# Optimization experiments

Measured on AMD Instinct MI355X. Metric: run time of the kernel, lower is better.

Reference implementation:

```python
import jax, jax.numpy as jnp
import numpy as np

N_NODES = 100000  # graph size (set via set_features/adj_lists in the original)
DEGREE = 32       # sampled neighbors per node (num_sample)
N_PAIRS = 8192    # link-prediction batch
FEAT_DIM = 9      # nn.Embedding(18, 9)
HID = 20          # enc1 embed_dim
OUT = 15          # n_out / enc2 embed_dim


def setup_inputs() -> dict:
    key = jax.random.key(0)
    ks = jax.random.split(key, 9)
    to_pred = jax.random.randint(ks[0], (N_PAIRS, 2), 0, N_NODES)
    adj = jax.random.randint(ks[1], (N_NODES, DEGREE), 0, N_NODES)
    feat = jax.random.normal(ks[2], (N_NODES, FEAT_DIM), dtype=jnp.float32)
    W1 = jax.random.normal(ks[3], (HID, 2 * FEAT_DIM), dtype=jnp.float32) * 0.1
    W2 = jax.random.normal(ks[4], (OUT, HID), dtype=jnp.float32) * 0.1
    fc1_w = jax.random.normal(ks[5], (15, 30), dtype=jnp.float32) * 0.1
    fc1_b = jnp.zeros((15,), dtype=jnp.float32)
    fc2_w = jax.random.normal(ks[6], (1, 15), dtype=jnp.float32) * 0.1
    fc2_b = jnp.zeros((1,), dtype=jnp.float32)
    return {"to_pred": to_pred, "adj": adj, "feat": feat, "W1": W1, "W2": W2,
            "fc1_w": fc1_w, "fc1_b": fc1_b, "fc2_w": fc2_w, "fc2_b": fc2_b}


def _enc1(nodes, feat, adj, W1):
    # GraphSAGE layer 1 (gcn=False): concat(self, mean(neighbors)) -> relu(W1 @ .)
    neigh_feat = feat[adj[nodes]].mean(axis=-2)          # [..., FEAT_DIM]
    combined = jnp.concatenate([feat[nodes], neigh_feat], axis=-1)  # [..., 2*FEAT_DIM]
    return jax.nn.relu(combined @ W1.T)                  # [..., HID]


def _enc2(nodes, feat, adj, W1, W2):
    # GraphSAGE layer 2 (gcn=True): neighbor set includes self, mean-only aggregate
    neighs = jnp.concatenate([adj[nodes], nodes[:, None]], axis=-1)  # [B, K+1]
    h1 = _enc1(neighs, feat, adj, W1)                    # [B, K+1, HID]
    return jax.nn.relu(h1.mean(axis=1) @ W2.T)           # [B, OUT]


def reference(to_pred, adj, feat, W1, W2, fc1_w, fc1_b, fc2_w, fc2_b):
    # two_fc_link_prediction: embed both endpoints, concat, 2-layer ReLU MLP
    e1 = _enc2(to_pred[:, 0], feat, adj, W1, W2)         # [B, OUT]
    e2 = _enc2(to_pred[:, 1], feat, adj, W1, W2)         # [B, OUT]
    cat = jnp.concatenate([e1, e2], axis=1)              # [B, 30]
    h = jax.nn.relu(cat @ fc1_w.T + fc1_b)               # [B, 15]
    out = jax.nn.relu(h @ fc2_w.T + fc2_b)               # [B, 1]
    return jnp.squeeze(out, axis=-1)                     # [B]
```

## Files before the change

### kernel.cpp

```cpp
#include <hip/hip_runtime.h>
#include <hip/hip_bf16.h>

#define N_NODES 100000
#define DEGREE 32
#define N_PAIRS 8192
#define FEAT 9
#define HID 20
#define NOUT 15

#define NPB 28
#define PPB 8

__global__ __launch_bounds__(256) void k_node_all(
    const int* __restrict__ adj,
    const float* __restrict__ feat,
    const float* __restrict__ W1,
    const float* __restrict__ W2,
    __hip_bfloat16* __restrict__ t_ws) {
  __shared__ float sW1[HID * 2 * FEAT];
  __shared__ float sW2[NOUT * HID];
  __shared__ float sComb[NPB][2 * FEAT];
  __shared__ float sH[NPB][HID];

  int tid = threadIdx.x;
  for (int i = tid; i < HID * 2 * FEAT; i += 256) sW1[i] = W1[i];
  for (int i = tid; i < NOUT * HID; i += 256) sW2[i] = W2[i];

  int base = blockIdx.x * NPB;

  if (tid < NPB * FEAT) {
    int nl = tid / FEAT;
    int j = tid - nl * FEAT;
    int n = base + nl;
    if (n < N_NODES) {
      const int4* arow4 = (const int4*)(adj + n * DEGREE);
      float s = 0.f;
#pragma unroll
      for (int c = 0; c < DEGREE / 4; ++c) {
        int4 a4 = arow4[c];
        s += feat[a4.x * FEAT + j];
        s += feat[a4.y * FEAT + j];
        s += feat[a4.z * FEAT + j];
        s += feat[a4.w * FEAT + j];
      }
      sComb[nl][j] = feat[n * FEAT + j];
      sComb[nl][FEAT + j] = s * (1.0f / DEGREE);
    }
  }
  __syncthreads();

  for (int idx = tid; idx < NPB * HID; idx += 256) {
    int nl = idx / HID;
    int i = idx - nl * HID;
    if (base + nl < N_NODES) {
      float acc = 0.f;
#pragma unroll
      for (int j = 0; j < 2 * FEAT; ++j) acc += sW1[i * 2 * FEAT + j] * sComb[nl][j];
      sH[nl][i] = fmaxf(acc, 0.f);
    }
  }
  __syncthreads();

  for (int idx = tid; idx < NPB * NOUT; idx += 256) {
    int nl = idx / NOUT;
    int d = idx - nl * NOUT;
    int n = base + nl;
    if (n < N_NODES) {
      float acc = 0.f;
#pragma unroll
      for (int i = 0; i < HID; ++i) acc += sW2[d * HID + i] * sH[nl][i];
      t_ws[n * NOUT + d] = __float2bfloat16(acc);
    }
  }
}

__global__ __launch_bounds__(256) void k_pair_all(
    const int* __restrict__ to_pred,
    const int* __restrict__ adj,
    const __hip_bfloat16* __restrict__ t_ws,
    const float* __restrict__ fc1_w,
    const float* __restrict__ fc1_b,
    const float* __restrict__ fc2_w,
    const float* __restrict__ fc2_b,
    float* __restrict__ out) {
  __shared__ float s1[15 * 30];
  __shared__ float b1v[15];
  __shared__ float s2v[15];
  __shared__ float b2v;
  __shared__ float sE[PPB][30];
  __shared__ float sHh[PPB][15];

  int tid = threadIdx.x;
  for (int i = tid; i < 15 * 30; i += 256) s1[i] = fc1_w[i];
  if (tid < 15) {
    b1v[tid] = fc1_b[tid];
    s2v[tid] = fc2_w[tid];
  }
  if (tid == 0) b2v = fc2_b[0];

  int pbase = blockIdx.x * PPB;

  if (tid < PPB * 30) {
    int pl = tid / 30;
    int slot = tid - pl * 30;
    int side = slot / 15;
    int d = slot - side * 15;
    int p = pbase + pl;
    int node = to_pred[2 * p + side];
    const int4* arow4 = (const int4*)(adj + node * DEGREE);
    float s = __bfloat162float(t_ws[node * NOUT + d]);
#pragma unroll
    for (int c = 0; c < DEGREE / 4; ++c) {
      int4 a4 = arow4[c];
      s += __bfloat162float(t_ws[a4.x * NOUT + d]);
      s += __bfloat162float(t_ws[a4.y * NOUT + d]);
      s += __bfloat162float(t_ws[a4.z * NOUT + d]);
      s += __bfloat162float(t_ws[a4.w * NOUT + d]);
    }
    sE[pl][slot] = fmaxf(s * (1.0f / (DEGREE + 1)), 0.f);
  }
  __syncthreads();

  if (tid < PPB * 15) {
    int pl = tid / 15;
    int i = tid - pl * 15;
    float acc = b1v[i];
#pragma unroll
    for (int j = 0; j < 30; ++j) acc += s1[i * 30 + j] * sE[pl][j];
    sHh[pl][i] = fmaxf(acc, 0.f);
  }
  __syncthreads();

  if (tid < PPB) {
    float acc = b2v;
#pragma unroll
    for (int i = 0; i < 15; ++i) acc += s2v[i] * sHh[tid][i];
    out[pbase + tid] = fmaxf(acc, 0.f);
  }
}

extern "C" void kernel_launch(void* const* d_in, const int* in_sizes, int n_in,
                              void* d_out, int out_size, void* d_ws,
                              size_t ws_size, hipStream_t stream) {
  const int* to_pred = (const int*)d_in[0];
  const int* adj     = (const int*)d_in[1];
  const float* feat  = (const float*)d_in[2];
  const float* W1    = (const float*)d_in[3];
  const float* W2    = (const float*)d_in[4];
  const float* fc1_w = (const float*)d_in[5];
  const float* fc1_b = (const float*)d_in[6];
  const float* fc2_w = (const float*)d_in[7];
  const float* fc2_b = (const float*)d_in[8];
  float* out         = (float*)d_out;

  __hip_bfloat16* t_ws = (__hip_bfloat16*)d_ws;

  int grid1 = (N_NODES + NPB - 1) / NPB;
  k_node_all<<<grid1, 256, 0, stream>>>(adj, feat, W1, W2, t_ws);

  int grid2 = N_PAIRS / PPB;
  k_pair_all<<<grid2, 256, 0, stream>>>(to_pred, adj, t_ws, fc1_w, fc1_b,
                                        fc2_w, fc2_b, out);
}
```

Baseline: 117.8 us.

## Pad features to bf16 rows and map neighbors to lanes with shuffle reductions

Adds a prep kernel that converts node features into 16-wide padded bf16 rows, so each neighbor gather becomes a single 16-byte vector load. The node and pair kernels are restructured so that each half-wave handles one node, with one lane per neighbor, and the neighbor sum is done with xor shuffles instead of per-feature scalar gathers. The intermediate table is padded to 16 bf16 per node for aligned vector loads. The cost is an extra kernel launch and pass over the features, more workspace, and bf16 rounding of the input features.

```diff
diff --git a/kernel.cpp b/kernel.cpp
--- a/kernel.cpp
+++ b/kernel.cpp
@@ -7,74 +7,94 @@
 #define FEAT 9
 #define HID 20
 #define NOUT 15
-
-#define NPB 28
-#define PPB 8
-
-__global__ __launch_bounds__(256) void k_node_all(
+#define FPAD 16
+
+__device__ __forceinline__ float bflo(unsigned int w) {
+  return __uint_as_float(w << 16);
+}
+__device__ __forceinline__ float bfhi(unsigned int w) {
+  return __uint_as_float(w & 0xffff0000u);
+}
+
+__global__ __launch_bounds__(256) void k_prep(
+    const float* __restrict__ feat, __hip_bfloat16* __restrict__ featb) {
+  int n = blockIdx.x * 256 + threadIdx.x;
+  if (n < N_NODES) {
+    const float* fr = feat + (size_t)n * FEAT;
+    __hip_bfloat16 u[FPAD];
+#pragma unroll
+    for (int j = 0; j < FEAT; ++j) u[j] = __float2bfloat16(fr[j]);
+#pragma unroll
+    for (int j = FEAT; j < FPAD; ++j) u[j] = __float2bfloat16(0.f);
+    uint4* dst = (uint4*)(featb + (size_t)n * FPAD);
+    dst[0] = *(const uint4*)(u);
+    dst[1] = *(const uint4*)(u + 8);
+  }
+}
+
+__global__ __launch_bounds__(256) void k_node(
     const int* __restrict__ adj,
     const float* __restrict__ feat,
+    const __hip_bfloat16* __restrict__ featb,
     const float* __restrict__ W1,
     const float* __restrict__ W2,
     __hip_bfloat16* __restrict__ t_ws) {
   __shared__ float sW1[HID * 2 * FEAT];
   __shared__ float sW2[NOUT * HID];
-  __shared__ float sComb[NPB][2 * FEAT];
-  __shared__ float sH[NPB][HID];
+  __shared__ float sH[4][2][HID];
 
   int tid = threadIdx.x;
   for (int i = tid; i < HID * 2 * FEAT; i += 256) sW1[i] = W1[i];
   for (int i = tid; i < NOUT * HID; i += 256) sW2[i] = W2[i];
-
-  int base = blockIdx.x * NPB;
-
-  if (tid < NPB * FEAT) {
-    int nl = tid / FEAT;
-    int j = tid - nl * FEAT;
-    int n = base + nl;
-    if (n < N_NODES) {
-      const int4* arow4 = (const int4*)(adj + n * DEGREE);
-      float s = 0.f;
-#pragma unroll
-      for (int c = 0; c < DEGREE / 4; ++c) {
-        int4 a4 = arow4[c];
-        s += feat[a4.x * FEAT + j];
-        s += feat[a4.y * FEAT + j];
-        s += feat[a4.z * FEAT + j];
-        s += feat[a4.w * FEAT + j];
-      }
-      sComb[nl][j] = feat[n * FEAT + j];
-      sComb[nl][FEAT + j] = s * (1.0f / DEGREE);
-    }
-  }
   __syncthreads();
 
-  for (int idx = tid; idx < NPB * HID; idx += 256) {
-    int nl = idx / HID;
-    int i = idx - nl * HID;
-    if (base + nl < N_NODES) {
-      float acc = 0.f;
-#pragma unroll
-      for (int j = 0; j < 2 * FEAT; ++j) acc += sW1[i * 2 * FEAT + j] * sComb[nl][j];
-      sH[nl][i] = fmaxf(acc, 0.f);
-    }
-  }
-  __syncthreads();
-
-  for (int idx = tid; idx < NPB * NOUT; idx += 256) {
-    int nl = idx / NOUT;
-    int d = idx - nl * NOUT;
-    int n = base + nl;
-    if (n < N_NODES) {
-      float acc = 0.f;
-#pragma unroll
-      for (int i = 0; i < HID; ++i) acc += sW2[d * HID + i] * sH[nl][i];
-      t_ws[n * NOUT + d] = __float2bfloat16(acc);
-    }
-  }
-}
-
-__global__ __launch_bounds__(256) void k_pair_all(
+  int wid = tid >> 6;
+  int lane = tid & 63;
+  int half = lane >> 5;
+  int k = lane & 31;
+  int node = blockIdx.x * 8 + wid * 2 + half;
+
+  int nbr = adj[(size_t)node * DEGREE + k];
+
+  const __hip_bfloat16* rp = featb + (size_t)nbr * FPAD;
+  uint4 r = *(const uint4*)rp;
+  unsigned short c8 = *(const unsigned short*)(rp + 8);
+
+  float v[FEAT];
+  v[0] = bflo(r.x); v[1] = bfhi(r.x);
+  v[2] = bflo(r.y); v[3] = bfhi(r.y);
+  v[4] = bflo(r.z); v[5] = bfhi(r.z);
+  v[6] = bflo(r.w); v[7] = bfhi(r.w);
+  v[8] = bflo((unsigned int)c8);
+
+#pragma unroll
+  for (int m = 1; m <= 16; m <<= 1) {
+#pragma unroll
+    for (int j = 0; j < FEAT; ++j) v[j] += __shfl_xor(v[j], m, 64);
+  }
+
+  if (k < HID) {
+    float self[FEAT];
+#pragma unroll
+    for (int j = 0; j < FEAT; ++j) self[j] = feat[(size_t)node * FEAT + j];
+    float acc = 0.f;
+#pragma unroll
+    for (int j = 0; j < FEAT; ++j) acc += sW1[k * 2 * FEAT + j] * self[j];
+#pragma unroll
+    for (int j = 0; j < FEAT; ++j)
+      acc += sW1[k * 2 * FEAT + FEAT + j] * (v[j] * (1.0f / DEGREE));
+    sH[wid][half][k] = fmaxf(acc, 0.f);
+  }
+  __builtin_amdgcn_wave_barrier();
+  if (k < NOUT) {
+    float acc = 0.f;
+#pragma unroll
+    for (int i = 0; i < HID; ++i) acc += sW2[k * HID + i] * sH[wid][half][i];
+    t_ws[(size_t)node * FPAD + k] = __float2bfloat16(acc);
+  }
+}
+
+__global__ __launch_bounds__(256) void k_pair(
     const int* __restrict__ to_pred,
     const int* __restrict__ adj,
     const __hip_bfloat16* __restrict__ t_ws,
@@ -87,8 +107,6 @@
   __shared__ float b1v[15];
   __shared__ float s2v[15];
   __shared__ float b2v;
-  __shared__ float sE[PPB][30];
-  __shared__ float sHh[PPB][15];
 
   int tid = threadIdx.x;
   for (int i = tid; i < 15 * 30; i += 256) s1[i] = fc1_w[i];
@@ -97,46 +115,67 @@
     s2v[tid] = fc2_w[tid];
   }
   if (tid == 0) b2v = fc2_b[0];
-
-  int pbase = blockIdx.x * PPB;
-
-  if (tid < PPB * 30) {
-    int pl = tid / 30;
-    int slot = tid - pl * 30;
-    int side = slot / 15;
-    int d = slot - side * 15;
-    int p = pbase + pl;
-    int node = to_pred[2 * p + side];
-    const int4* arow4 = (const int4*)(adj + node * DEGREE);
-    float s = __bfloat162float(t_ws[node * NOUT + d]);
-#pragma unroll
-    for (int c = 0; c < DEGREE / 4; ++c) {
-      int4 a4 = arow4[c];
-      s += __bfloat162float(t_ws[a4.x * NOUT + d]);
-      s += __bfloat162float(t_ws[a4.y * NOUT + d]);
-      s += __bfloat162float(t_ws[a4.z * NOUT + d]);
-      s += __bfloat162float(t_ws[a4.w * NOUT + d]);
-    }
-    sE[pl][slot] = fmaxf(s * (1.0f / (DEGREE + 1)), 0.f);
-  }
   __syncthreads();
 
-  if (tid < PPB * 15) {
-    int pl = tid / 15;
-    int i = tid - pl * 15;
-    float acc = b1v[i];
-#pragma unroll
-    for (int j = 0; j < 30; ++j) acc += s1[i * 30 + j] * sE[pl][j];
-    sHh[pl][i] = fmaxf(acc, 0.f);
-  }
-  __syncthreads();
-
-  if (tid < PPB) {
-    float acc = b2v;
-#pragma unroll
-    for (int i = 0; i < 15; ++i) acc += s2v[i] * sHh[tid][i];
-    out[pbase + tid] = fmaxf(acc, 0.f);
-  }
+  int wid = tid >> 6;
+  int lane = tid & 63;
+  int half = lane >> 5;
+  int k = lane & 31;
+  int pair = blockIdx.x * 4 + wid;
+  int node = to_pred[2 * pair + half];
+
+  int nbr = adj[(size_t)node * DEGREE + k];
+  const __hip_bfloat16* rp = t_ws + (size_t)nbr * FPAD;
+  uint4 a = *(const uint4*)rp;
+  uint4 b = *(const uint4*)(rp + 8);
+
+  float w[NOUT];
+  w[0] = bflo(a.x);  w[1] = bfhi(a.x);
+  w[2] = bflo(a.y);  w[3] = bfhi(a.y);
+  w[4] = bflo(a.z);  w[5] = bfhi(a.z);
+  w[6] = bflo(a.w);  w[7] = bfhi(a.w);
+  w[8] = bflo(b.x);  w[9] = bfhi(b.x);
+  w[10] = bflo(b.y); w[11] = bfhi(b.y);
+  w[12] = bflo(b.z); w[13] = bfhi(b.z);
+  w[14] = bflo(b.w);
+
+#pragma unroll
+  for (int m = 1; m <= 16; m <<= 1) {
+#pragma unroll
+    for (int j = 0; j < NOUT; ++j) w[j] += __shfl_xor(w[j], m, 64);
+  }
+
+  const __hip_bfloat16* sp = t_ws + (size_t)node * FPAD;
+  uint4 sa = *(const uint4*)sp;
+  uint4 sb = *(const uint4*)(sp + 8);
+  float e[NOUT];
+  {
+    float sv[NOUT];
+    sv[0] = bflo(sa.x);  sv[1] = bfhi(sa.x);
+    sv[2] = bflo(sa.y);  sv[3] = bfhi(sa.y);
+    sv[4] = bflo(sa.z);  sv[5] = bfhi(sa.z);
+    sv[6] = bflo(sa.w);  sv[7] = bfhi(sa.w);
+    sv[8] = bflo(sb.x);  sv[9] = bfhi(sb.x);
+    sv[10] = bflo(sb.y); sv[11] = bfhi(sb.y);
+    sv[12] = bflo(sb.z); sv[13] = bfhi(sb.z);
+    sv[14] = bflo(sb.w);
+#pragma unroll
+    for (int j = 0; j < NOUT; ++j)
+      e[j] = fmaxf((w[j] + sv[j]) * (1.0f / (DEGREE + 1)), 0.f);
+  }
+
+  float p = (k < 15 && half == 0) ? b1v[k] : 0.f;
+  if (k < 15) {
+#pragma unroll
+    for (int j = 0; j < 15; ++j) p += s1[k * 30 + half * 15 + j] * e[j];
+  }
+  float pOther = __shfl_xor(p, 32, 64);
+  float h = fmaxf(p + pOther, 0.f);
+
+  float q = (k < 15) ? s2v[k] * h : 0.f;
+#pragma unroll
+  for (int m = 1; m <= 16; m <<= 1) q += __shfl_xor(q, m, 64);
+  if (lane == 0) out[pair] = fmaxf(b2v + q, 0.f);
 }
 
 extern "C" void kernel_launch(void* const* d_in, const int* in_sizes, int n_in,
@@ -153,12 +192,16 @@
   const float* fc2_b = (const float*)d_in[8];
   float* out         = (float*)d_out;
 
-  __hip_bfloat16* t_ws = (__hip_bfloat16*)d_ws;
-
-  int grid1 = (N_NODES + NPB - 1) / NPB;
-  k_node_all<<<grid1, 256, 0, stream>>>(adj, feat, W1, W2, t_ws);
-
-  int grid2 = N_PAIRS / PPB;
-  k_pair_all<<<grid2, 256, 0, stream>>>(to_pred, adj, t_ws, fc1_w, fc1_b,
-                                        fc2_w, fc2_b, out);
-}
+  __hip_bfloat16* featb = (__hip_bfloat16*)d_ws;
+  __hip_bfloat16* t_ws  = featb + (size_t)N_NODES * FPAD;
+
+  int grid0 = (N_NODES + 255) / 256;
+  k_prep<<<grid0, 256, 0, stream>>>(feat, featb);
+
+  int grid1 = N_NODES / 8;
+  k_node<<<grid1, 256, 0, stream>>>(adj, feat, featb, W1, W2, t_ws);
+
+  int grid2 = N_PAIRS / 4;
+  k_pair<<<grid2, 256, 0, stream>>>(to_pred, adj, t_ws, fc1_w, fc1_b,
+                                    fc2_w, fc2_b, out);
+}
```

After: 130.9 us. 1.11x slower.

## Process multiple node/pair chunks per block and pad node table rows to 16

Applied to the files above, without the earlier changes.

Each block of both kernels now loops over four chunks of nodes or pairs instead of one, amortizing the shared-memory weight loads across more work and launching four times fewer blocks. The bf16 per-node intermediate is stored with a row stride of 16 instead of 15, so each row is 32-byte aligned for the second kernel's gathers. The extra per-chunk barriers serialize chunks inside a block, and the smaller grid cuts the parallelism available to hide gather latency.

```diff
diff --git a/kernel.cpp b/kernel.cpp
--- a/kernel.cpp
+++ b/kernel.cpp
@@ -7,9 +7,12 @@
 #define FEAT 9
 #define HID 20
 #define NOUT 15
+#define FPAD 16
 
 #define NPB 28
+#define NCH1 4
 #define PPB 8
+#define NCH2 4
 
 __global__ __launch_bounds__(256) void k_node_all(
     const int* __restrict__ adj,
@@ -26,51 +29,57 @@
   for (int i = tid; i < HID * 2 * FEAT; i += 256) sW1[i] = W1[i];
   for (int i = tid; i < NOUT * HID; i += 256) sW2[i] = W2[i];
 
-  int base = blockIdx.x * NPB;
+  int bbase = blockIdx.x * (NPB * NCH1);
 
-  if (tid < NPB * FEAT) {
-    int nl = tid / FEAT;
-    int j = tid - nl * FEAT;
-    int n = base + nl;
-    if (n < N_NODES) {
-      const int4* arow4 = (const int4*)(adj + n * DEGREE);
-      float s = 0.f;
+  for (int ch = 0; ch < NCH1; ++ch) {
+    int base = bbase + ch * NPB;
+
+    if (tid < NPB * FEAT) {
+      int nl = tid / FEAT;
+      int j = tid - nl * FEAT;
+      int n = base + nl;
+      if (n < N_NODES) {
+        const int4* arow4 = (const int4*)(adj + (size_t)n * DEGREE);
+        float s = 0.f;
 #pragma unroll
-      for (int c = 0; c < DEGREE / 4; ++c) {
-        int4 a4 = arow4[c];
-        s += feat[a4.x * FEAT + j];
-        s += feat[a4.y * FEAT + j];
-        s += feat[a4.z * FEAT + j];
-        s += feat[a4.w * FEAT + j];
+        for (int c = 0; c < DEGREE / 4; ++c) {
+          int4 a4 = arow4[c];
+          s += feat[(size_t)a4.x * FEAT + j];
+          s += feat[(size_t)a4.y * FEAT + j];
+          s += feat[(size_t)a4.z * FEAT + j];
+          s += feat[(size_t)a4.w * FEAT + j];
+        }
+        sComb[nl][j] = feat[(size_t)n * FEAT + j];
+        sComb[nl][FEAT + j] = s * (1.0f / DEGREE);
       }
-      sComb[nl][j] = feat[n * FEAT + j];
-      sComb[nl][FEAT + j] = s * (1.0f / DEGREE);
     }
-  }
-  __syncthreads();
+    __syncthreads();
 
-  for (int idx = tid; idx < NPB * HID; idx += 256) {
-    int nl = idx / HID;
-    int i = idx - nl * HID;
-    if (base + nl < N_NODES) {
-      float acc = 0.f;
+    for (int idx = tid; idx < NPB * HID; idx += 256) {
+      int nl = idx / HID;
+      int i = idx - nl * HID;
+      if (base + nl < N_NODES) {
+        float acc = 0.f;
 #pragma unroll
-      for (int j = 0; j < 2 * FEAT; ++j) acc += sW1[i * 2 * FEAT + j] * sComb[nl][j];
-      sH[nl][i] = fmaxf(acc, 0.f);
+        for (int j = 0; j < 2 * FEAT; ++j)
+          acc += sW1[i * 2 * FEAT + j] * sComb[nl][j];
+        sH[nl][i] = fmaxf(acc, 0.f);
+      }
     }
-  }
-  __syncthreads();
+    __syncthreads();
 
-  for (int idx = tid; idx < NPB * NOUT; idx += 256) {
-    int nl = idx / NOUT;
-    int d = idx - nl * NOUT;
-    int n = base + nl;
-    if (n < N_NODES) {
-      float acc = 0.f;
+    for (int idx = tid; idx < NPB * NOUT; idx += 256) {
+      int nl = idx / NOUT;
+      int d = idx - nl * NOUT;
+      int n = base + nl;
+      if (n < N_NODES) {
+        float acc = 0.f;
 #pragma unroll
-      for (int i = 0; i < HID; ++i) acc += sW2[d * HID + i] * sH[nl][i];
-      t_ws[n * NOUT + d] = __float2bfloat16(acc);
+        for (int i = 0; i < HID; ++i) acc += sW2[d * HID + i] * sH[nl][i];
+        t_ws[(size_t)n * FPAD + d] = __float2bfloat16(acc);
+      }
     }
+    __syncthreads();
   }
 }
 
@@ -98,44 +107,49 @@
   }
   if (tid == 0) b2v = fc2_b[0];
 
-  int pbase = blockIdx.x * PPB;
+  int bbase = blockIdx.x * (PPB * NCH2);
 
-  if (tid < PPB * 30) {
-    int pl = tid / 30;
-    int slot = tid - pl * 30;
-    int side = slot / 15;
-    int d = slot - side * 15;
-    int p = pbase + pl;
-    int node = to_pred[2 * p + side];
-    const int4* arow4 = (const int4*)(adj + node * DEGREE);
-    float s = __bfloat162float(t_ws[node * NOUT + d]);
+  for (int ch = 0; ch < NCH2; ++ch) {
+    int pbase = bbase + ch * PPB;
+
+    if (tid < PPB * 30) {
+      int pl = tid / 30;
+      int slot = tid - pl * 30;
+      int side = slot / 15;
+      int d = slot - side * 15;
+      int p = pbase + pl;
+      int node = to_pred[2 * p + side];
+      const int4* arow4 = (const int4*)(adj + (size_t)node * DEGREE);
+      float s = __bfloat162float(t_ws[(size_t)node * FPAD + d]);
 #pragma unroll
-    for (int c = 0; c < DEGREE / 4; ++c) {
-      int4 a4 = arow4[c];
-      s += __bfloat162float(t_ws[a4.x * NOUT + d]);
-      s += __bfloat162float(t_ws[a4.y * NOUT + d]);
-      s += __bfloat162float(t_ws[a4.z * NOUT + d]);
-      s += __bfloat162float(t_ws[a4.w * NOUT + d]);
+      for (int c = 0; c < DEGREE / 4; ++c) {
+        int4 a4 = arow4[c];
+        s += __bfloat162float(t_ws[(size_t)a4.x * FPAD + d]);
+        s += __bfloat162float(t_ws[(size_t)a4.y * FPAD + d]);
+        s += __bfloat162float(t_ws[(size_t)a4.z * FPAD + d]);
+        s += __bfloat162float(t_ws[(size_t)a4.w * FPAD + d]);
+      }
+      sE[pl][slot] = fmaxf(s * (1.0f / (DEGREE + 1)), 0.f);
     }
-    sE[pl][slot] = fmaxf(s * (1.0f / (DEGREE + 1)), 0.f);
-  }
-  __syncthreads();
+    __syncthreads();
 
-  if (tid < PPB * 15) {
-    int pl = tid / 15;
-    int i = tid - pl * 15;
-    float acc = b1v[i];
+    if (tid < PPB * 15) {
+      int pl = tid / 15;
+      int i = tid - pl * 15;
+      float acc = b1v[i];
 #pragma unroll
-    for (int j = 0; j < 30; ++j) acc += s1[i * 30 + j] * sE[pl][j];
-    sHh[pl][i] = fmaxf(acc, 0.f);
-  }
-  __syncthreads();
+      for (int j = 0; j < 30; ++j) acc += s1[i * 30 + j] * sE[pl][j];
+      sHh[pl][i] = fmaxf(acc, 0.f);
+    }
+    __syncthreads();
 
-  if (tid < PPB) {
-    float acc = b2v;
+    if (tid < PPB) {
+      float acc = b2v;
 #pragma unroll
-    for (int i = 0; i < 15; ++i) acc += s2v[i] * sHh[tid][i];
-    out[pbase + tid] = fmaxf(acc, 0.f);
+      for (int i = 0; i < 15; ++i) acc += s2v[i] * sHh[tid][i];
+      out[pbase + tid] = fmaxf(acc, 0.f);
+    }
+    __syncthreads();
   }
 }
 
@@ -155,10 +169,10 @@
 
   __hip_bfloat16* t_ws = (__hip_bfloat16*)d_ws;
 
-  int grid1 = (N_NODES + NPB - 1) / NPB;
+  int grid1 = (N_NODES + NPB * NCH1 - 1) / (NPB * NCH1);
   k_node_all<<<grid1, 256, 0, stream>>>(adj, feat, W1, W2, t_ws);
 
-  int grid2 = N_PAIRS / PPB;
+  int grid2 = N_PAIRS / (PPB * NCH2);
   k_pair_all<<<grid2, 256, 0, stream>>>(to_pred, adj, t_ws, fc1_w, fc1_b,
                                         fc2_w, fc2_b, out);
 }
```

New measurement: 138.8 us. 17.9% more time.
